# Optimization experiments

Measured on AMD Instinct MI355X. Metric: run time of the kernel, lower is better.

## Reference

```python
import jax, jax.numpy as jnp
import numpy as np

B, N0, N1, N2, HS, NCLS = 16384, 57, 20, 10, 5, 17
EPS = 1e-4  # SPDRectified eigenvalue floor
_TRI = np.triu_indices(HS)  # upper-tri vectorization indices


def _bilinear(x, W):
    # SPDTransform: W^T X W, W: (in, out) column-orthonormal (Stiefel)
    return jnp.einsum('ji,bjk,kl->bil', W, x, W)


def _rectify(x):
    # SPDRectified: eigh, clamp eigenvalues at EPS, recompose
    w, v = jnp.linalg.eigh(x)
    w = jnp.maximum(w, EPS)
    return jnp.einsum('bij,bj,bkj->bik', v, w, v)


def _logmap(x):
    # SPDTangentSpace log map: eigh, log eigenvalues, recompose
    w, v = jnp.linalg.eigh(x)
    w = jnp.log(w)
    return jnp.einsum('bij,bj,bkj->bik', v, w, v)


def setup_inputs() -> dict:
    key = jax.random.key(0)
    ks = jax.random.split(key, 6)
    A = jax.random.normal(ks[0], (B, N0, N0), dtype=jnp.float32)
    # SPD input: A A^T / N0 + 0.01 I
    x = jnp.einsum('bij,bkj->bik', A, A) / N0 + 0.01 * jnp.eye(N0, dtype=jnp.float32)

    def stiefel(k, m, n):
        q, _ = jnp.linalg.qr(jax.random.normal(k, (m, n), dtype=jnp.float32))
        return q  # (m, n) column-orthonormal

    W1 = stiefel(ks[1], N0, N1)
    W2 = stiefel(ks[2], N1, N2)
    W3 = stiefel(ks[3], N2, HS)
    tri = HS * (HS + 1) // 2
    lin_w = jax.random.normal(ks[4], (NCLS, tri), dtype=jnp.float32) / np.sqrt(tri)
    lin_b = jax.random.normal(ks[5], (NCLS,), dtype=jnp.float32) * 0.01
    return {"x": x, "W1": W1, "W2": W2, "W3": W3, "lin_w": lin_w, "lin_b": lin_b}


def reference(x, W1, W2, W3, lin_w, lin_b):
    x = _rectify(_bilinear(x, W1))   # [B,20,20]
    x = _rectify(_bilinear(x, W2))   # [B,10,10]
    x = _rectify(_bilinear(x, W3))   # [B,HS,HS]
    x = _logmap(x)                   # tangent space
    vec = x[:, _TRI[0], _TRI[1]]     # [B, HS*(HS+1)/2]
    return vec @ lin_w.T + lin_b     # [B, 17]
```

## Files before the change

kernel.cpp:

```cpp
#include <hip/hip_runtime.h>
#include <math.h>

#define BATCH 16384
#define N0 57
#define NX 3249
#define HS 5
#define NCLS 17
#define NTRI 15
#define EPSV 1e-4f

template<int CTRL>
__device__ __forceinline__ float dpp_mov0(float x) {
    return __int_as_float(__builtin_amdgcn_update_dpp(
        0, __float_as_int(x), CTRL, 0xF, 0xF, true));
}
__device__ __forceinline__ float wave_sum64(float x) {
    x += dpp_mov0<0x111>(x);
    x += dpp_mov0<0x112>(x);
    x += dpp_mov0<0x114>(x);
    x += dpp_mov0<0x118>(x);
    x += dpp_mov0<0x142>(x);
    x += dpp_mov0<0x143>(x);
    return x;
}

__device__ __forceinline__ float frcp(float x)  { return __builtin_amdgcn_rcpf(x); }
__device__ __forceinline__ float frsq(float x)  { return __builtin_amdgcn_rsqf(x); }
__device__ __forceinline__ float fsqrt(float x) { return __builtin_amdgcn_sqrtf(x); }

__global__ __launch_bounds__(128) void k_setup(const float* __restrict__ W1,
                                               const float* __restrict__ W2,
                                               const float* __restrict__ W3,
                                               float* __restrict__ wc_out) {
    __shared__ float w23[100];
    int t = threadIdx.x;
    if (t < 100) {
        int k = t / 5, j = t % 5;
        float acc = 0.f;
        for (int l = 0; l < 10; ++l) acc = fmaf(W2[k * 10 + l], W3[l * 5 + j], acc);
        w23[t] = acc;
    }
    __syncthreads();
    if (t < N0) {
        float r[5];
        #pragma unroll
        for (int j = 0; j < 5; ++j) {
            float acc = 0.f;
            for (int k = 0; k < 20; ++k) acc = fmaf(W1[t * 20 + k], w23[k * 5 + j], acc);
            r[j] = acc;
        }
        float4* o = (float4*)&wc_out[t * 8];
        o[0] = make_float4(r[0], r[1], r[2], r[3]);
        o[1] = make_float4(r[4], 0.f, 0.f, 0.f);
    }
}

__global__ __launch_bounds__(256, 8) void k_main(const float* __restrict__ x,
                                                 const float* __restrict__ wc,
                                                 float* __restrict__ y_out) {
    const int tid  = threadIdx.x;
    const int lane = tid & 63;
    const int wave = tid >> 6;
    const int m    = blockIdx.x * 4 + wave;

    float wv[HS];
    {
        int a = (lane < N0) ? lane : 0;
        const float4* wp = (const float4*)&wc[a * 8];
        float4 v0 = wp[0];
        float  v4 = wc[a * 8 + 4];
        wv[0] = v0.x; wv[1] = v0.y; wv[2] = v0.z; wv[3] = v0.w; wv[4] = v4;
        if (lane >= N0) { wv[0] = wv[1] = wv[2] = wv[3] = wv[4] = 0.f; }
    }

    const int lc = (lane < N0) ? lane : 56;
    const float* base = x + (size_t)m * NX + lc;
    float s[HS] = {0.f, 0.f, 0.f, 0.f, 0.f};
    #pragma unroll
    for (int b = 0; b < N0; ++b) {
        float xv = base[b * N0];
        #pragma unroll
        for (int j = 0; j < HS; ++j) s[j] = fmaf(xv, wc[b * 8 + j], s[j]);
    }

    float p[NTRI];
    int u = 0;
    #pragma unroll
    for (int i = 0; i < HS; ++i)
        #pragma unroll
        for (int j = i; j < HS; ++j) { p[u] = wave_sum64(wv[i] * s[j]); ++u; }

    if (lane == 63) {
        float4* o = (float4*)&y_out[(size_t)m * 16];
        o[0] = make_float4(p[0],  p[1],  p[2],  p[3]);
        o[1] = make_float4(p[4],  p[5],  p[6],  p[7]);
        o[2] = make_float4(p[8],  p[9],  p[10], p[11]);
        o[3] = make_float4(p[12], p[13], p[14], 0.f);
    }
}

__global__ __launch_bounds__(64) void k_eig(const float* __restrict__ y_in,
                                            const float* __restrict__ lin_w,
                                            const float* __restrict__ lin_b,
                                            float* __restrict__ out) {
    int m = blockIdx.x * 64 + threadIdx.x;
    const float4* yin = (const float4*)&y_in[(size_t)m * 16];
    float4 q0 = yin[0], q1 = yin[1], q2 = yin[2], q3 = yin[3];
    float tri[16] = {q0.x, q0.y, q0.z, q0.w, q1.x, q1.y, q1.z, q1.w,
                     q2.x, q2.y, q2.z, q2.w, q3.x, q3.y, q3.z, q3.w};

    float A[HS][HS], V[HS][HS];
    int t = 0;
    #pragma unroll
    for (int i = 0; i < HS; ++i)
        #pragma unroll
        for (int j = i; j < HS; ++j) { A[i][j] = tri[t]; A[j][i] = tri[t]; ++t; }
    #pragma unroll
    for (int i = 0; i < HS; ++i)
        #pragma unroll
        for (int j = 0; j < HS; ++j) V[i][j] = (i == j) ? 1.f : 0.f;

    #pragma unroll
    for (int sweep = 0; sweep < 6; ++sweep) {
        #pragma unroll
        for (int p = 0; p < HS - 1; ++p) {
            #pragma unroll
            for (int q = p + 1; q < HS; ++q) {
                float apq = A[p][q];
                float app = A[p][p], aqq = A[q][q];
                bool nz = fabsf(apq) > 1e-30f;
                float theta = (aqq - app) * 0.5f * frcp(apq);
                float tt = frcp(fabsf(theta) + fsqrt(fmaf(theta, theta, 1.f)));
                tt = copysignf(tt, theta);
                tt = nz ? tt : 0.f;
                float c = frsq(fmaf(tt, tt, 1.f));
                float sn = tt * c;
                #pragma unroll
                for (int k = 0; k < HS; ++k) {
                    float akp = A[k][p], akq = A[k][q];
                    A[k][p] = fmaf(c, akp, -sn * akq);
                    A[k][q] = fmaf(sn, akp,  c * akq);
                }
                #pragma unroll
                for (int k = 0; k < HS; ++k) {
                    float apk = A[p][k], aqk = A[q][k];
                    A[p][k] = fmaf(c, apk, -sn * aqk);
                    A[q][k] = fmaf(sn, apk,  c * aqk);
                }
                #pragma unroll
                for (int k = 0; k < HS; ++k) {
                    float vkp = V[k][p], vkq = V[k][q];
                    V[k][p] = fmaf(c, vkp, -sn * vkq);
                    V[k][q] = fmaf(sn, vkp,  c * vkq);
                }
            }
        }
    }

    float lwv[HS];
    #pragma unroll
    for (int i = 0; i < HS; ++i)
        lwv[i] = 0.69314718056f * __log2f(fmaxf(A[i][i], EPSV));

    float tri2[NTRI];
    t = 0;
    #pragma unroll
    for (int i = 0; i < HS; ++i) {
        float vi[HS];
        #pragma unroll
        for (int k = 0; k < HS; ++k) vi[k] = V[i][k] * lwv[k];
        #pragma unroll
        for (int j = i; j < HS; ++j) {
            float acc = 0.f;
            #pragma unroll
            for (int k = 0; k < HS; ++k) acc = fmaf(vi[k], V[j][k], acc);
            tri2[t++] = acc;
        }
    }

    #pragma unroll
    for (int c = 0; c < NCLS; ++c) {
        float acc = lin_b[c];
        #pragma unroll
        for (int k = 0; k < NTRI; ++k) acc = fmaf(tri2[k], lin_w[c * NTRI + k], acc);
        out[(size_t)m * NCLS + c] = acc;
    }
}

extern "C" void kernel_launch(void* const* d_in, const int* in_sizes, int n_in,
                              void* d_out, int out_size, void* d_ws, size_t ws_size,
                              hipStream_t stream) {
    const float* x     = (const float*)d_in[0];
    const float* W1    = (const float*)d_in[1];
    const float* W2    = (const float*)d_in[2];
    const float* W3    = (const float*)d_in[3];
    const float* lin_w = (const float*)d_in[4];
    const float* lin_b = (const float*)d_in[5];
    float* out = (float*)d_out;
    float* ws  = (float*)d_ws;
    float* wc  = ws;
    float* y   = ws + 512;

    k_setup<<<1, 128, 0, stream>>>(W1, W2, W3, wc);
    k_main<<<BATCH / 4, 256, 0, stream>>>(x, wc, y);
    k_eig<<<BATCH / 64, 64, 0, stream>>>(y, lin_w, lin_b, out);
}
```

Baseline: 52.78 us.

## Fuse weight-composition setup into main kernel and process multiple matrices per block

```diff
diff --git a/kernel.cpp b/kernel.cpp
--- a/kernel.cpp
+++ b/kernel.cpp
@@ -8,6 +8,7 @@
 #define NCLS 17
 #define NTRI 15
 #define EPSV 1e-4f
+#define MPB 16
 
 template<int CTRL>
 __device__ __forceinline__ float dpp_mov0(float x) {
@@ -28,74 +29,71 @@
 __device__ __forceinline__ float frsq(float x)  { return __builtin_amdgcn_rsqf(x); }
 __device__ __forceinline__ float fsqrt(float x) { return __builtin_amdgcn_sqrtf(x); }
 
-__global__ __launch_bounds__(128) void k_setup(const float* __restrict__ W1,
-                                               const float* __restrict__ W2,
-                                               const float* __restrict__ W3,
-                                               float* __restrict__ wc_out) {
+__global__ __launch_bounds__(256) void k_main(const float* __restrict__ x,
+                                              const float* __restrict__ W1,
+                                              const float* __restrict__ W2,
+                                              const float* __restrict__ W3,
+                                              float* __restrict__ y_out) {
     __shared__ float w23[100];
-    int t = threadIdx.x;
-    if (t < 100) {
-        int k = t / 5, j = t % 5;
-        float acc = 0.f;
-        for (int l = 0; l < 10; ++l) acc = fmaf(W2[k * 10 + l], W3[l * 5 + j], acc);
-        w23[t] = acc;
-    }
-    __syncthreads();
-    if (t < N0) {
-        float r[5];
-        #pragma unroll
-        for (int j = 0; j < 5; ++j) {
-            float acc = 0.f;
-            for (int k = 0; k < 20; ++k) acc = fmaf(W1[t * 20 + k], w23[k * 5 + j], acc);
-            r[j] = acc;
-        }
-        float4* o = (float4*)&wc_out[t * 8];
-        o[0] = make_float4(r[0], r[1], r[2], r[3]);
-        o[1] = make_float4(r[4], 0.f, 0.f, 0.f);
-    }
-}
-
-__global__ __launch_bounds__(256, 8) void k_main(const float* __restrict__ x,
-                                                 const float* __restrict__ wc,
-                                                 float* __restrict__ y_out) {
+    __shared__ float wcs[N0 * 8];
     const int tid  = threadIdx.x;
     const int lane = tid & 63;
     const int wave = tid >> 6;
-    const int m    = blockIdx.x * 4 + wave;
+
+    if (tid < 100) {
+        int k = tid / 5, j = tid % 5;
+        float acc = 0.f;
+        #pragma unroll
+        for (int l = 0; l < 10; ++l) acc = fmaf(W2[k * 10 + l], W3[l * 5 + j], acc);
+        w23[tid] = acc;
+    }
+    __syncthreads();
+    if (tid < N0) {
+        #pragma unroll
+        for (int j = 0; j < 5; ++j) {
+            float acc = 0.f;
+            #pragma unroll
+            for (int k = 0; k < 20; ++k) acc = fmaf(W1[tid * 20 + k], w23[k * 5 + j], acc);
+            wcs[tid * 8 + j] = acc;
+        }
+    }
+    __syncthreads();
 
     float wv[HS];
     {
         int a = (lane < N0) ? lane : 0;
-        const float4* wp = (const float4*)&wc[a * 8];
-        float4 v0 = wp[0];
-        float  v4 = wc[a * 8 + 4];
-        wv[0] = v0.x; wv[1] = v0.y; wv[2] = v0.z; wv[3] = v0.w; wv[4] = v4;
+        #pragma unroll
+        for (int i = 0; i < HS; ++i) wv[i] = wcs[a * 8 + i];
         if (lane >= N0) { wv[0] = wv[1] = wv[2] = wv[3] = wv[4] = 0.f; }
     }
 
     const int lc = (lane < N0) ? lane : 56;
-    const float* base = x + (size_t)m * NX + lc;
-    float s[HS] = {0.f, 0.f, 0.f, 0.f, 0.f};
-    #pragma unroll
-    for (int b = 0; b < N0; ++b) {
-        float xv = base[b * N0];
-        #pragma unroll
-        for (int j = 0; j < HS; ++j) s[j] = fmaf(xv, wc[b * 8 + j], s[j]);
-    }
-
-    float p[NTRI];
-    int u = 0;
-    #pragma unroll
-    for (int i = 0; i < HS; ++i)
-        #pragma unroll
-        for (int j = i; j < HS; ++j) { p[u] = wave_sum64(wv[i] * s[j]); ++u; }
-
-    if (lane == 63) {
-        float4* o = (float4*)&y_out[(size_t)m * 16];
-        o[0] = make_float4(p[0],  p[1],  p[2],  p[3]);
-        o[1] = make_float4(p[4],  p[5],  p[6],  p[7]);
-        o[2] = make_float4(p[8],  p[9],  p[10], p[11]);
-        o[3] = make_float4(p[12], p[13], p[14], 0.f);
+    for (int it = 0; it < MPB / 4; ++it) {
+        const int m = blockIdx.x * MPB + it * 4 + wave;
+        const float* base = x + (size_t)m * NX + lc;
+
+        float s[HS] = {0.f, 0.f, 0.f, 0.f, 0.f};
+        #pragma unroll
+        for (int b = 0; b < N0; ++b) {
+            float xv = base[b * N0];
+            #pragma unroll
+            for (int j = 0; j < HS; ++j) s[j] = fmaf(xv, wcs[b * 8 + j], s[j]);
+        }
+
+        float p[NTRI];
+        int u = 0;
+        #pragma unroll
+        for (int i = 0; i < HS; ++i)
+            #pragma unroll
+            for (int j = i; j < HS; ++j) { p[u] = wave_sum64(wv[i] * s[j]); ++u; }
+
+        if (lane == 63) {
+            float4* o = (float4*)&y_out[(size_t)m * 16];
+            o[0] = make_float4(p[0],  p[1],  p[2],  p[3]);
+            o[1] = make_float4(p[4],  p[5],  p[6],  p[7]);
+            o[2] = make_float4(p[8],  p[9],  p[10], p[11]);
+            o[3] = make_float4(p[12], p[13], p[14], 0.f);
+        }
     }
 }
 
@@ -121,7 +119,7 @@
         for (int j = 0; j < HS; ++j) V[i][j] = (i == j) ? 1.f : 0.f;
 
     #pragma unroll
-    for (int sweep = 0; sweep < 6; ++sweep) {
+    for (int sweep = 0; sweep < 5; ++sweep) {
         #pragma unroll
         for (int p = 0; p < HS - 1; ++p) {
             #pragma unroll
@@ -197,11 +195,8 @@
     const float* lin_w = (const float*)d_in[4];
     const float* lin_b = (const float*)d_in[5];
     float* out = (float*)d_out;
-    float* ws  = (float*)d_ws;
-    float* wc  = ws;
-    float* y   = ws + 512;
-
-    k_setup<<<1, 128, 0, stream>>>(W1, W2, W3, wc);
-    k_main<<<BATCH / 4, 256, 0, stream>>>(x, wc, y);
+    float* y   = (float*)d_ws;
+
+    k_main<<<BATCH / MPB, 256, 0, stream>>>(x, W1, W2, W3, y);
     k_eig<<<BATCH / 64, 64, 0, stream>>>(y, lin_w, lin_b, out);
 }
```

After: 75.83 us. 43.7% more time.
